# Performance work log

Measured on AMD Instinct MI355X. Metric: run time of the kernel, lower is better.

## Reference

```python
import jax, jax.numpy as jnp
import numpy as np
import math

B, L, P, D, H, RBF = 4, 256, 1024, 512, 8, 50
d = D // H  # head_dim = 64
EPS = 1e-5


def setup_inputs() -> dict:
    key = jax.random.key(0)
    ks = jax.random.split(key, 20)
    s = 1.0 / math.sqrt(D)
    inp = {
        "query": jax.random.normal(ks[0], (B, L, D), jnp.float32),
        "key": jax.random.normal(ks[1], (B, P, D), jnp.float32),
        "value": jax.random.normal(ks[2], (B, P, D), jnp.float32),
        "cross_rbf": jax.random.uniform(ks[3], (B, L, P, RBF), jnp.float32),
        "key_mask": jax.random.randint(ks[4], (B, P), 0, 2, jnp.int32),
        "Wq": jax.random.normal(ks[5], (D, D), jnp.float32) * s,
        "bq": jnp.zeros((D,), jnp.float32),
        "Wk": jax.random.normal(ks[6], (D, D), jnp.float32) * s,
        "bk": jnp.zeros((D,), jnp.float32),
        "Wv": jax.random.normal(ks[7], (D, D), jnp.float32) * s,
        "bv": jnp.zeros((D,), jnp.float32),
        "Wr": jax.random.normal(ks[8], (RBF, H), jnp.float32) * (1.0 / math.sqrt(RBF)),
        "br": jnp.zeros((H,), jnp.float32),
        "Wo": jax.random.normal(ks[9], (D, D), jnp.float32) * s,
        "bo": jnp.zeros((D,), jnp.float32),
        "gamma": jnp.ones((D,), jnp.float32),
        "beta": jnp.zeros((D,), jnp.float32),
    }
    return inp


def reference(query, key, value, cross_rbf, key_mask,
              Wq, bq, Wk, bk, Wv, bv, Wr, br, Wo, bo, gamma, beta):
    Q = (query @ Wq + bq).reshape(B, L, H, d)
    K = (key @ Wk + bk).reshape(B, P, H, d)
    V = (value @ Wv + bv).reshape(B, P, H, d)
    # scores [B, L, P, H]
    attn = jnp.einsum('blhd,bphd->blph', Q, K) / math.sqrt(d)
    dist_bias = cross_rbf @ Wr + br  # [B, L, P, H]
    attn = attn + dist_bias
    attn = jnp.where(key_mask[:, None, :, None] == 0, -1e9, attn)
    attn = jax.nn.softmax(attn, axis=2)  # softmax over P
    out = jnp.einsum('blph,bphd->blhd', attn, V).reshape(B, L, D)
    out = out @ Wo + bo
    x = query + out
    mu = jnp.mean(x, axis=-1, keepdims=True)
    var = jnp.mean((x - mu) ** 2, axis=-1, keepdims=True)
    normed = (x - mu) / jnp.sqrt(var + EPS) * gamma + beta
    return normed, attn.mean(axis=-1)
```

## Files before the change

### kernel.cpp

```cpp
#include <hip/hip_runtime.h>
#include <hip/hip_bf16.h>

#define BB 4
#define LL 256
#define PP 1024
#define DD 512
#define HH 8
#define HD 64
#define NRBF 50

__device__ __forceinline__ float bf2f(unsigned short u) {
  return __uint_as_float((unsigned)u << 16);
}

__device__ __forceinline__ float ldf(const void* p, size_t i, bool f32) {
  if (f32) return ((const float*)p)[i];
  return bf2f(((const unsigned short*)p)[i]);
}

__device__ __forceinline__ float4 ld4e(const void* p, size_t i, bool f32) {
  if (f32) return *(const float4*)((const float*)p + i);
  ushort4 u = *(const ushort4*)((const unsigned short*)p + i);
  float4 r;
  r.x = bf2f(u.x); r.y = bf2f(u.y); r.z = bf2f(u.z); r.w = bf2f(u.w);
  return r;
}

__global__ __launch_bounds__(256) void detect_dtype(const float* q, int* flag) {
  __shared__ int cnt;
  if (threadIdx.x == 0) cnt = 0;
  __syncthreads();
  int c = 0;
  for (int i = threadIdx.x; i < 1024; i += 256) {
    unsigned u = __float_as_uint(q[i]);
    unsigned e = (u >> 23) & 0xffu;
    if (e >= 104u && e <= 140u) c++;
  }
  atomicAdd(&cnt, c);
  __syncthreads();
  if (threadIdx.x == 0) *flag = (cnt > 512) ? 1 : 0;
}

__device__ void gemm128(const void* __restrict__ X, const void* __restrict__ W,
                        const void* __restrict__ bias, float* __restrict__ Y,
                        const int bm, const int bn, const int mode,
                        const bool f32, float* lds) {
  const int tid = threadIdx.x;
  const int tx = tid & 15, ty = tid >> 4;
  const int lr = tid >> 1, lc = (tid & 1) * 8;
  const int wk = tid >> 5, wc = (tid & 31) * 4;
  float acc[8][8] = {};
  float4 ra0, ra1, rb0, rb1;

  ra0 = ld4e(X, (size_t)(bm + lr) * 512 + lc, f32);
  ra1 = ld4e(X, (size_t)(bm + lr) * 512 + lc + 4, f32);
  rb0 = ld4e(W, (size_t)wk * 512 + bn + wc, f32);
  rb1 = ld4e(W, (size_t)(wk + 8) * 512 + bn + wc, f32);
  {
    float* Ab = lds;
    float* Bb = lds + 4096;
    Ab[(lc + 0) * 128 + lr] = ra0.x; Ab[(lc + 1) * 128 + lr] = ra0.y;
    Ab[(lc + 2) * 128 + lr] = ra0.z; Ab[(lc + 3) * 128 + lr] = ra0.w;
    Ab[(lc + 4) * 128 + lr] = ra1.x; Ab[(lc + 5) * 128 + lr] = ra1.y;
    Ab[(lc + 6) * 128 + lr] = ra1.z; Ab[(lc + 7) * 128 + lr] = ra1.w;
    *(float4*)&Bb[wk * 128 + wc] = rb0;
    *(float4*)&Bb[(wk + 8) * 128 + wc] = rb1;
  }
  __syncthreads();

  int buf = 0;
  for (int tt = 0; tt < 32; ++tt) {
    if (tt < 31) {
      const int k0 = (tt + 1) * 16;
      ra0 = ld4e(X, (size_t)(bm + lr) * 512 + k0 + lc, f32);
      ra1 = ld4e(X, (size_t)(bm + lr) * 512 + k0 + lc + 4, f32);
      rb0 = ld4e(W, (size_t)(k0 + wk) * 512 + bn + wc, f32);
      rb1 = ld4e(W, (size_t)(k0 + wk + 8) * 512 + bn + wc, f32);
    }
    {
      const float* Ab = lds + buf * 2048;
      const float* Bb = lds + 4096 + buf * 2048;
#pragma unroll
      for (int k = 0; k < 16; ++k) {
        float4 aL = *(const float4*)&Ab[k * 128 + ty * 4];
        float4 aH = *(const float4*)&Ab[k * 128 + 64 + ty * 4];
        float4 bL = *(const float4*)&Bb[k * 128 + tx * 4];
        float4 bH = *(const float4*)&Bb[k * 128 + 64 + tx * 4];
        const float a8[8] = {aL.x, aL.y, aL.z, aL.w, aH.x, aH.y, aH.z, aH.w};
        const float b8[8] = {bL.x, bL.y, bL.z, bL.w, bH.x, bH.y, bH.z, bH.w};
#pragma unroll
        for (int i = 0; i < 8; ++i)
#pragma unroll
          for (int j = 0; j < 8; ++j)
            acc[i][j] = fmaf(a8[i], b8[j], acc[i][j]);
      }
    }
    if (tt < 31) {
      float* Ab = lds + (buf ^ 1) * 2048;
      float* Bb = lds + 4096 + (buf ^ 1) * 2048;
      Ab[(lc + 0) * 128 + lr] = ra0.x; Ab[(lc + 1) * 128 + lr] = ra0.y;
      Ab[(lc + 2) * 128 + lr] = ra0.z; Ab[(lc + 3) * 128 + lr] = ra0.w;
      Ab[(lc + 4) * 128 + lr] = ra1.x; Ab[(lc + 5) * 128 + lr] = ra1.y;
      Ab[(lc + 6) * 128 + lr] = ra1.z; Ab[(lc + 7) * 128 + lr] = ra1.w;
      *(float4*)&Bb[wk * 128 + wc] = rb0;
      *(float4*)&Bb[(wk + 8) * 128 + wc] = rb1;
    }
    __syncthreads();
    buf ^= 1;
  }

  if (mode == 0) {
#pragma unroll
    for (int rh = 0; rh < 2; ++rh)
#pragma unroll
      for (int i = 0; i < 4; ++i) {
        const int r = bm + rh * 64 + ty * 4 + i;
#pragma unroll
        for (int ch = 0; ch < 2; ++ch) {
          const int c = bn + ch * 64 + tx * 4;
          float4 o;
          o.x = acc[rh * 4 + i][ch * 4 + 0] + ldf(bias, c + 0, f32);
          o.y = acc[rh * 4 + i][ch * 4 + 1] + ldf(bias, c + 1, f32);
          o.z = acc[rh * 4 + i][ch * 4 + 2] + ldf(bias, c + 2, f32);
          o.w = acc[rh * 4 + i][ch * 4 + 3] + ldf(bias, c + 3, f32);
          *(float4*)&Y[(size_t)r * 512 + c] = o;
        }
      }
  } else {
    const int bq = bm >> 10;
    const int pb = bm & 1023;
#pragma unroll
    for (int ch = 0; ch < 2; ++ch)
#pragma unroll
      for (int j = 0; j < 4; ++j) {
        const int c = bn + ch * 64 + tx * 4 + j;
        const float bb = ldf(bias, c, f32);
#pragma unroll
        for (int rh = 0; rh < 2; ++rh) {
          float4 pv;
          pv.x = acc[rh * 4 + 0][ch * 4 + j] + bb;
          pv.y = acc[rh * 4 + 1][ch * 4 + j] + bb;
          pv.z = acc[rh * 4 + 2][ch * 4 + j] + bb;
          pv.w = acc[rh * 4 + 3][ch * 4 + j] + bb;
          const int p0 = pb + rh * 64 + ty * 4;
          *(float4*)&Y[(((size_t)bq * 8 + (c >> 6)) * 64 + (c & 63)) * 1024 +
                       p0] = pv;
        }
      }
  }
}

__global__ __launch_bounds__(256) void qkv_gemm(
    const void* __restrict__ query, const void* __restrict__ key,
    const void* __restrict__ value, const void* __restrict__ Wq,
    const void* __restrict__ bq_, const void* __restrict__ Wk,
    const void* __restrict__ bk_, const void* __restrict__ Wv,
    const void* __restrict__ bv_, float* __restrict__ Qw,
    float* __restrict__ Ktw, float* __restrict__ Vw,
    const int* __restrict__ flag) {
  __shared__ float lds[8192];
  const bool f32 = (*flag != 0);
  const int blk = blockIdx.x;

  const void *X, *W, *bias;
  float* Y;
  int mode, mi, ni;
  if (blk < 32) {
    X = query; W = Wq; bias = bq_; Y = Qw; mode = 0;
    mi = blk >> 2; ni = blk & 3;
  } else if (blk < 160) {
    const int q2 = blk - 32;
    X = key; W = Wk; bias = bk_; Y = Ktw; mode = 1;
    mi = q2 >> 2; ni = q2 & 3;
  } else {
    const int q2 = blk - 160;
    X = value; W = Wv; bias = bv_; Y = Vw; mode = 0;
    mi = q2 >> 2; ni = q2 & 3;
  }
  gemm128(X, W, bias, Y, mi * 128, ni * 128, mode, f32, lds);
}

#define SST 1028

__global__ __launch_bounds__(512) void attn_v10(
    const float* __restrict__ Q,
    const float* __restrict__ Kt,
    const float* __restrict__ V,
    const void* __restrict__ rbf,
    const void* __restrict__ Wr,
    const void* __restrict__ br_,
    const int* __restrict__ mask,
    float* __restrict__ AO,
    void* __restrict__ d_out, const int* __restrict__ flag) {
  const int xcd = blockIdx.x & 7;
  const int idx = blockIdx.x >> 3;
  const int b = xcd >> 1;
  const int lq = ((xcd & 1) << 5) | idx;
  const int bl0 = b * LL + lq * 4;
  const int t = threadIdx.x;
  const bool f32 = (*flag != 0);

  __shared__ float qS[4][512];
  __shared__ float wrS[NRBF * 8];
  __shared__ float brS[8];
  __shared__ float scoresS[4][8 * SST];

  for (int i = t; i < 2048; i += 512)
    qS[i >> 9][i & 511] = Q[(size_t)bl0 * 512 + i];
  for (int i = t; i < NRBF * 8; i += 512) wrS[i] = ldf(Wr, i, f32);
  if (t < 8) brS[t] = ldf(br_, t, f32);
  __syncthreads();

  {
    const int qh = t >> 8;
    const int tq = t & 255;
#pragma unroll
    for (int qi = 0; qi < 2; ++qi) {
      const int q = qh * 2 + qi;
      float acc[4][8];
#pragma unroll
      for (int e = 0; e < 4; ++e)
#pragma unroll
        for (int h = 0; h < 8; ++h) acc[e][h] = brS[h];
      const size_t rbase = ((size_t)(bl0 + q) * 1024 + 4 * tq) * NRBF;
      if (f32) {
        const float* rowb = (const float*)rbf + rbase;
#pragma unroll
        for (int e = 0; e < 4; ++e) {
          const float2* rp = (const float2*)(rowb + e * NRBF);
#pragma unroll 5
          for (int j = 0; j < 25; ++j) {
            const float2 r2 = rp[j];
            const float4 wa = *(const float4*)&wrS[(2 * j) * 8];
            const float4 wb = *(const float4*)&wrS[(2 * j) * 8 + 4];
            const float4 wc = *(const float4*)&wrS[(2 * j + 1) * 8];
            const float4 wd = *(const float4*)&wrS[(2 * j + 1) * 8 + 4];
            acc[e][0] = fmaf(r2.x, wa.x, acc[e][0]);
            acc[e][1] = fmaf(r2.x, wa.y, acc[e][1]);
            acc[e][2] = fmaf(r2.x, wa.z, acc[e][2]);
            acc[e][3] = fmaf(r2.x, wa.w, acc[e][3]);
            acc[e][4] = fmaf(r2.x, wb.x, acc[e][4]);
            acc[e][5] = fmaf(r2.x, wb.y, acc[e][5]);
            acc[e][6] = fmaf(r2.x, wb.z, acc[e][6]);
            acc[e][7] = fmaf(r2.x, wb.w, acc[e][7]);
            acc[e][0] = fmaf(r2.y, wc.x, acc[e][0]);
            acc[e][1] = fmaf(r2.y, wc.y, acc[e][1]);
            acc[e][2] = fmaf(r2.y, wc.z, acc[e][2]);
            acc[e][3] = fmaf(r2.y, wc.w, acc[e][3]);
            acc[e][4] = fmaf(r2.y, wd.x, acc[e][4]);
            acc[e][5] = fmaf(r2.y, wd.y, acc[e][5]);
            acc[e][6] = fmaf(r2.y, wd.z, acc[e][6]);
            acc[e][7] = fmaf(r2.y, wd.w, acc[e][7]);
          }
        }
      } else {
        const unsigned short* rb = (const unsigned short*)rbf + rbase;
#pragma unroll
        for (int e = 0; e < 4; ++e) {
#pragma unroll 1
          for (int j = 0; j < 50; ++j) {
            const float rv = bf2f(rb[e * 50 + j]);
#pragma unroll
            for (int h = 0; h < 8; ++h)
              acc[e][h] = fmaf(rv, wrS[j * 8 + h], acc[e][h]);
          }
        }
      }
#pragma unroll
      for (int h = 0; h < 8; ++h) {
        float4 o;
        o.x = acc[0][h]; o.y = acc[1][h]; o.z = acc[2][h]; o.w = acc[3][h];
        *(float4*)&scoresS[q][h * SST + 4 * tq] = o;
      }
    }
  }
  __syncthreads();

  {
    const int tq = t & 255;
    const int hh = t >> 8;
    const int4 mk4 = *(const int4*)(mask + b * PP + 4 * tq);
#pragma unroll 1
    for (int hi = 0; hi < 4; ++hi) {
      const int h = hh * 4 + hi;
      const float4* ktp =
          (const float4*)(Kt + ((size_t)b * 8 + h) * 64 * 1024) + tq;
      float4 a0 = {0.f, 0.f, 0.f, 0.f}, a1 = {0.f, 0.f, 0.f, 0.f};
      float4 a2 = {0.f, 0.f, 0.f, 0.f}, a3 = {0.f, 0.f, 0.f, 0.f};
#pragma unroll 2
      for (int dq = 0; dq < 16; ++dq) {
        float4 q0 = *(const float4*)&qS[0][h * 64 + dq * 4];
        float4 q1 = *(const float4*)&qS[1][h * 64 + dq * 4];
        float4 q2 = *(const float4*)&qS[2][h * 64 + dq * 4];
        float4 q3 = *(const float4*)&qS[3][h * 64 + dq * 4];
        float4 k0 = ktp[(size_t)(dq * 4 + 0) * 256];
        float4 k1 = ktp[(size_t)(dq * 4 + 1) * 256];
        float4 k2 = ktp[(size_t)(dq * 4 + 2) * 256];
        float4 k3 = ktp[(size_t)(dq * 4 + 3) * 256];
        a0.x = fmaf(q0.x, k0.x, a0.x); a0.y = fmaf(q0.x, k0.y, a0.y);
        a0.z = fmaf(q0.x, k0.z, a0.z); a0.w = fmaf(q0.x, k0.w, a0.w);
        a0.x = fmaf(q0.y, k1.x, a0.x); a0.y = fmaf(q0.y, k1.y, a0.y);
        a0.z = fmaf(q0.y, k1.z, a0.z); a0.w = fmaf(q0.y, k1.w, a0.w);
        a0.x = fmaf(q0.z, k2.x, a0.x); a0.y = fmaf(q0.z, k2.y, a0.y);
        a0.z = fmaf(q0.z, k2.z, a0.z); a0.w = fmaf(q0.z, k2.w, a0.w);
        a0.x = fmaf(q0.w, k3.x, a0.x); a0.y = fmaf(q0.w, k3.y, a0.y);
        a0.z = fmaf(q0.w, k3.z, a0.z); a0.w = fmaf(q0.w, k3.w, a0.w);
        a1.x = fmaf(q1.x, k0.x, a1.x); a1.y = fmaf(q1.x, k0.y, a1.y);
        a1.z = fmaf(q1.x, k0.z, a1.z); a1.w = fmaf(q1.x, k0.w, a1.w);
        a1.x = fmaf(q1.y, k1.x, a1.x); a1.y = fmaf(q1.y, k1.y, a1.y);
        a1.z = fmaf(q1.y, k1.z, a1.z); a1.w = fmaf(q1.y, k1.w, a1.w);
        a1.x = fmaf(q1.z, k2.x, a1.x); a1.y = fmaf(q1.z, k2.y, a1.y);
        a1.z = fmaf(q1.z, k2.z, a1.z); a1.w = fmaf(q1.z, k2.w, a1.w);
        a1.x = fmaf(q1.w, k3.x, a1.x); a1.y = fmaf(q1.w, k3.y, a1.y);
        a1.z = fmaf(q1.w, k3.z, a1.z); a1.w = fmaf(q1.w, k3.w, a1.w);
        a2.x = fmaf(q2.x, k0.x, a2.x); a2.y = fmaf(q2.x, k0.y, a2.y);
        a2.z = fmaf(q2.x, k0.z, a2.z); a2.w = fmaf(q2.x, k0.w, a2.w);
        a2.x = fmaf(q2.y, k1.x, a2.x); a2.y = fmaf(q2.y, k1.y, a2.y);
        a2.z = fmaf(q2.y, k1.z, a2.z); a2.w = fmaf(q2.y, k1.w, a2.w);
        a2.x = fmaf(q2.z, k2.x, a2.x); a2.y = fmaf(q2.z, k2.y, a2.y);
        a2.z = fmaf(q2.z, k2.z, a2.z); a2.w = fmaf(q2.z, k2.w, a2.w);
        a2.x = fmaf(q2.w, k3.x, a2.x); a2.y = fmaf(q2.w, k3.y, a2.y);
        a2.z = fmaf(q2.w, k3.z, a2.z); a2.w = fmaf(q2.w, k3.w, a2.w);
        a3.x = fmaf(q3.x, k0.x, a3.x); a3.y = fmaf(q3.x, k0.y, a3.y);
        a3.z = fmaf(q3.x, k0.z, a3.z); a3.w = fmaf(q3.x, k0.w, a3.w);
        a3.x = fmaf(q3.y, k1.x, a3.x); a3.y = fmaf(q3.y, k1.y, a3.y);
        a3.z = fmaf(q3.y, k1.z, a3.z); a3.w = fmaf(q3.y, k1.w, a3.w);
        a3.x = fmaf(q3.z, k2.x, a3.x); a3.y = fmaf(q3.z, k2.y, a3.y);
        a3.z = fmaf(q3.z, k2.z, a3.z); a3.w = fmaf(q3.z, k2.w, a3.w);
        a3.x = fmaf(q3.w, k3.x, a3.x); a3.y = fmaf(q3.w, k3.y, a3.y);
        a3.z = fmaf(q3.w, k3.z, a3.z); a3.w = fmaf(q3.w, k3.w, a3.w);
      }
      float4 av[4] = {a0, a1, a2, a3};
#pragma unroll
      for (int qi = 0; qi < 4; ++qi) {
        float4 bq4 = *(const float4*)&scoresS[qi][h * SST + 4 * tq];
        float4 s;
        s.x = (mk4.x == 0) ? -1e9f : fmaf(av[qi].x, 0.125f, bq4.x);
        s.y = (mk4.y == 0) ? -1e9f : fmaf(av[qi].y, 0.125f, bq4.y);
        s.z = (mk4.z == 0) ? -1e9f : fmaf(av[qi].z, 0.125f, bq4.z);
        s.w = (mk4.w == 0) ? -1e9f : fmaf(av[qi].w, 0.125f, bq4.w);
        *(float4*)&scoresS[qi][h * SST + 4 * tq] = s;
      }
    }
  }
  __syncthreads();

  {
    const int wave = t >> 6, lane = t & 63;
    for (int pr = wave * 4; pr < wave * 4 + 4; ++pr) {
      float* sc = &scoresS[pr >> 3][(pr & 7) * SST];
      float m = -3.0e38f;
      for (int i = lane; i < PP; i += 64) m = fmaxf(m, sc[i]);
#pragma unroll
      for (int off = 32; off; off >>= 1) m = fmaxf(m, __shfl_xor(m, off, 64));
      float sum = 0.f;
      for (int i = lane; i < PP; i += 64) {
        float e = __expf(sc[i] - m);
        sc[i] = e;
        sum += e;
      }
#pragma unroll
      for (int off = 32; off; off >>= 1) sum += __shfl_xor(sum, off, 64);
      const float inv = 1.0f / sum;
      for (int i = lane; i < PP; i += 64) sc[i] *= inv;
    }
  }
  __syncthreads();

  for (int w = t; w < 1024; w += 512) {
    const int q = w >> 8, pq = w & 255;
    float4 s = {0.f, 0.f, 0.f, 0.f};
#pragma unroll
    for (int h = 0; h < 8; ++h) {
      float4 v = *(const float4*)&scoresS[q][h * SST + 4 * pq];
      s.x += v.x; s.y += v.y; s.z += v.z; s.w += v.w;
    }
    s.x *= 0.125f; s.y *= 0.125f; s.z *= 0.125f; s.w *= 0.125f;
    const size_t base =
        (size_t)BB * LL * DD + (size_t)(bl0 + q) * PP + 4 * pq;
    if (f32) {
      *(float4*)((float*)d_out + base) = s;
    } else {
      __hip_bfloat16* o1 = (__hip_bfloat16*)d_out;
      o1[base + 0] = __float2bfloat16(s.x);
      o1[base + 1] = __float2bfloat16(s.y);
      o1[base + 2] = __float2bfloat16(s.z);
      o1[base + 3] = __float2bfloat16(s.w);
    }
  }

  float4 pa[4];
  {
    const int cq = t & 127;
    const int ph = t >> 7;
    const int h = cq >> 4;
    const float* sc0 = &scoresS[0][h * SST];
    const float* sc1 = &scoresS[1][h * SST];
    const float* sc2 = &scoresS[2][h * SST];
    const float* sc3 = &scoresS[3][h * SST];
    const float4* Vb = (const float4*)(V + (size_t)b * PP * 512) + cq;
    float4 A0 = {0.f, 0.f, 0.f, 0.f}, A1 = {0.f, 0.f, 0.f, 0.f};
    float4 A2 = {0.f, 0.f, 0.f, 0.f}, A3 = {0.f, 0.f, 0.f, 0.f};
    const int p0 = ph * 256;
#pragma unroll 2
    for (int p4 = p0; p4 < p0 + 256; p4 += 4) {
      float4 pr0 = *(const float4*)&sc0[p4];
      float4 pr1 = *(const float4*)&sc1[p4];
      float4 pr2 = *(const float4*)&sc2[p4];
      float4 pr3 = *(const float4*)&sc3[p4];
      float4 v0 = Vb[(size_t)(p4 + 0) * 128];
      float4 v1 = Vb[(size_t)(p4 + 1) * 128];
      float4 v2 = Vb[(size_t)(p4 + 2) * 128];
      float4 v3 = Vb[(size_t)(p4 + 3) * 128];
      A0.x = fmaf(pr0.x, v0.x, A0.x); A0.y = fmaf(pr0.x, v0.y, A0.y);
      A0.z = fmaf(pr0.x, v0.z, A0.z); A0.w = fmaf(pr0.x, v0.w, A0.w);
      A0.x = fmaf(pr0.y, v1.x, A0.x); A0.y = fmaf(pr0.y, v1.y, A0.y);
      A0.z = fmaf(pr0.y, v1.z, A0.z); A0.w = fmaf(pr0.y, v1.w, A0.w);
      A0.x = fmaf(pr0.z, v2.x, A0.x); A0.y = fmaf(pr0.z, v2.y, A0.y);
      A0.z = fmaf(pr0.z, v2.z, A0.z); A0.w = fmaf(pr0.z, v2.w, A0.w);
      A0.x = fmaf(pr0.w, v3.x, A0.x); A0.y = fmaf(pr0.w, v3.y, A0.y);
      A0.z = fmaf(pr0.w, v3.z, A0.z); A0.w = fmaf(pr0.w, v3.w, A0.w);
      A1.x = fmaf(pr1.x, v0.x, A1.x); A1.y = fmaf(pr1.x, v0.y, A1.y);
      A1.z = fmaf(pr1.x, v0.z, A1.z); A1.w = fmaf(pr1.x, v0.w, A1.w);
      A1.x = fmaf(pr1.y, v1.x, A1.x); A1.y = fmaf(pr1.y, v1.y, A1.y);
      A1.z = fmaf(pr1.y, v1.z, A1.z); A1.w = fmaf(pr1.y, v1.w, A1.w);
      A1.x = fmaf(pr1.z, v2.x, A1.x); A1.y = fmaf(pr1.z, v2.y, A1.y);
      A1.z = fmaf(pr1.z, v2.z, A1.z); A1.w = fmaf(pr1.z, v2.w, A1.w);
      A1.x = fmaf(pr1.w, v3.x, A1.x); A1.y = fmaf(pr1.w, v3.y, A1.y);
      A1.z = fmaf(pr1.w, v3.z, A1.z); A1.w = fmaf(pr1.w, v3.w, A1.w);
      A2.x = fmaf(pr2.x, v0.x, A2.x); A2.y = fmaf(pr2.x, v0.y, A2.y);
      A2.z = fmaf(pr2.x, v0.z, A2.z); A2.w = fmaf(pr2.x, v0.w, A2.w);
      A2.x = fmaf(pr2.y, v1.x, A2.x); A2.y = fmaf(pr2.y, v1.y, A2.y);
      A2.z = fmaf(pr2.y, v1.z, A2.z); A2.w = fmaf(pr2.y, v1.w, A2.w);
      A2.x = fmaf(pr2.z, v2.x, A2.x); A2.y = fmaf(pr2.z, v2.y, A2.y);
      A2.z = fmaf(pr2.z, v2.z, A2.z); A2.w = fmaf(pr2.z, v2.w, A2.w);
      A2.x = fmaf(pr2.w, v3.x, A2.x); A2.y = fmaf(pr2.w, v3.y, A2.y);
      A2.z = fmaf(pr2.w, v3.z, A2.z); A2.w = fmaf(pr2.w, v3.w, A2.w);
      A3.x = fmaf(pr3.x, v0.x, A3.x); A3.y = fmaf(pr3.x, v0.y, A3.y);
      A3.z = fmaf(pr3.x, v0.z, A3.z); A3.w = fmaf(pr3.x, v0.w, A3.w);
      A3.x = fmaf(pr3.y, v1.x, A3.x); A3.y = fmaf(pr3.y, v1.y, A3.y);
      A3.z = fmaf(pr3.y, v1.z, A3.z); A3.w = fmaf(pr3.y, v1.w, A3.w);
      A3.x = fmaf(pr3.z, v2.x, A3.x); A3.y = fmaf(pr3.z, v2.y, A3.y);
      A3.z = fmaf(pr3.z, v2.z, A3.z); A3.w = fmaf(pr3.z, v2.w, A3.w);
      A3.x = fmaf(pr3.w, v3.x, A3.x); A3.y = fmaf(pr3.w, v3.y, A3.y);
      A3.z = fmaf(pr3.w, v3.z, A3.z); A3.w = fmaf(pr3.w, v3.w, A3.w);
    }
    pa[0] = A0; pa[1] = A1; pa[2] = A2; pa[3] = A3;
  }
  __syncthreads();
  {
    const int cq = t & 127, ph = t >> 7;
    float* parts = &scoresS[0][0];
#pragma unroll
    for (int qi = 0; qi < 4; ++qi)
      *(float4*)&parts[((qi * 4 + ph) * 128 + cq) * 4] = pa[qi];
  }
  __syncthreads();
  {
    const int q = t >> 7, c = t & 127;
    const float* parts = &scoresS[0][0];
    float4 a = *(const float4*)&parts[((q * 4 + 0) * 128 + c) * 4];
#pragma unroll
    for (int ph = 1; ph < 4; ++ph) {
      float4 x = *(const float4*)&parts[((q * 4 + ph) * 128 + c) * 4];
      a.x += x.x; a.y += x.y; a.z += x.z; a.w += x.w;
    }
    *(float4*)&AO[(size_t)(bl0 + q) * 512 + 4 * c] = a;
  }
}

__global__ __launch_bounds__(256) void proj_out(
    const float* __restrict__ X, const void* __restrict__ W,
    const void* __restrict__ bias, const void* __restrict__ resid,
    float* __restrict__ Y, const int* __restrict__ flag) {
  __shared__ float As[16][64];
  __shared__ float Bs[16][64];
  const bool f32 = (*flag != 0);
  const int bm = blockIdx.x * 64, bn = blockIdx.y * 64;
  const int tid = threadIdx.x;
  const int tx = tid & 15, ty = tid >> 4;
  float acc[4][4] = {};
  for (int k0 = 0; k0 < 512; k0 += 16) {
    {
      int r = tid >> 2, kf = (tid & 3) * 4;
      float4 x4 = *(const float4*)(X + (size_t)(bm + r) * 512 + k0 + kf);
      As[kf + 0][r] = x4.x; As[kf + 1][r] = x4.y;
      As[kf + 2][r] = x4.z; As[kf + 3][r] = x4.w;
    }
    if (f32) {
      int kk = tid >> 4, cf = (tid & 15) * 4;
      *(float4*)&Bs[kk][cf] =
          *(const float4*)((const float*)W + (size_t)(k0 + kk) * 512 + bn + cf);
    } else {
      const unsigned short* Wb = (const unsigned short*)W;
      for (int f = tid; f < 16 * 64; f += 256) {
        int kk = f >> 6, c = f & 63;
        Bs[kk][c] = bf2f(Wb[(size_t)(k0 + kk) * 512 + bn + c]);
      }
    }
    __syncthreads();
#pragma unroll
    for (int k = 0; k < 16; ++k) {
      float4 a4 = *(const float4*)&As[k][ty * 4];
      float4 b4 = *(const float4*)&Bs[k][tx * 4];
      acc[0][0] = fmaf(a4.x, b4.x, acc[0][0]); acc[0][1] = fmaf(a4.x, b4.y, acc[0][1]);
      acc[0][2] = fmaf(a4.x, b4.z, acc[0][2]); acc[0][3] = fmaf(a4.x, b4.w, acc[0][3]);
      acc[1][0] = fmaf(a4.y, b4.x, acc[1][0]); acc[1][1] = fmaf(a4.y, b4.y, acc[1][1]);
      acc[1][2] = fmaf(a4.y, b4.z, acc[1][2]); acc[1][3] = fmaf(a4.y, b4.w, acc[1][3]);
      acc[2][0] = fmaf(a4.z, b4.x, acc[2][0]); acc[2][1] = fmaf(a4.z, b4.y, acc[2][1]);
      acc[2][2] = fmaf(a4.z, b4.z, acc[2][2]); acc[2][3] = fmaf(a4.z, b4.w, acc[2][3]);
      acc[3][0] = fmaf(a4.w, b4.x, acc[3][0]); acc[3][1] = fmaf(a4.w, b4.y, acc[3][1]);
      acc[3][2] = fmaf(a4.w, b4.z, acc[3][2]); acc[3][3] = fmaf(a4.w, b4.w, acc[3][3]);
    }
    __syncthreads();
  }
#pragma unroll
  for (int i = 0; i < 4; ++i) {
    int r = bm + ty * 4 + i;
    float4 o;
#pragma unroll
    for (int j = 0; j < 4; ++j) {
      int c = bn + tx * 4 + j;
      float v = acc[i][j] + ldf(bias, c, f32) +
                ldf(resid, (size_t)r * 512 + c, f32);
      ((float*)&o)[j] = v;
    }
    *(float4*)(Y + (size_t)r * 512 + bn + tx * 4) = o;
  }
}

__global__ __launch_bounds__(256) void ln_kernel(
    const float* __restrict__ Xw, const void* __restrict__ gamma,
    const void* __restrict__ beta, void* __restrict__ d_out,
    const int* __restrict__ flag) {
  const int bl = blockIdx.x;
  const int tid = threadIdx.x;
  const bool f32 = (*flag != 0);
  __shared__ float red[16];
  float v0 = Xw[(size_t)bl * 512 + tid];
  float v1 = Xw[(size_t)bl * 512 + tid + 256];
  float s = v0 + v1, s2 = v0 * v0 + v1 * v1;
#pragma unroll
  for (int off = 32; off; off >>= 1) {
    s += __shfl_xor(s, off, 64);
    s2 += __shfl_xor(s2, off, 64);
  }
  const int wave = tid >> 6, lane = tid & 63;
  if (lane == 0) { red[wave] = s; red[8 + wave] = s2; }
  __syncthreads();
  if (tid == 0) {
    float ts = 0.f, ts2 = 0.f;
    for (int w = 0; w < 4; ++w) { ts += red[w]; ts2 += red[8 + w]; }
    red[0] = ts; red[1] = ts2;
  }
  __syncthreads();
  const float mu = red[0] * (1.0f / 512.0f);
  const float var = red[1] * (1.0f / 512.0f) - mu * mu;
  const float rstd = rsqrtf(var + 1e-5f);
  float o0 = (v0 - mu) * rstd * ldf(gamma, tid, f32) + ldf(beta, tid, f32);
  float o1 = (v1 - mu) * rstd * ldf(gamma, tid + 256, f32) +
             ldf(beta, tid + 256, f32);
  if (f32) {
    float* o = (float*)d_out;
    o[(size_t)bl * 512 + tid] = o0;
    o[(size_t)bl * 512 + tid + 256] = o1;
  } else {
    __hip_bfloat16* o = (__hip_bfloat16*)d_out;
    o[(size_t)bl * 512 + tid] = __float2bfloat16(o0);
    o[(size_t)bl * 512 + tid + 256] = __float2bfloat16(o1);
  }
}

extern "C" void kernel_launch(void* const* d_in, const int* in_sizes, int n_in,
                              void* d_out, int out_size, void* d_ws,
                              size_t ws_size, hipStream_t stream) {
  const void* query = d_in[0];
  const void* key = d_in[1];
  const void* value = d_in[2];
  const void* rbf = d_in[3];
  const int* key_mask = (const int*)d_in[4];
  const void* Wq = d_in[5];
  const void* bq = d_in[6];
  const void* Wk = d_in[7];
  const void* bk = d_in[8];
  const void* Wv = d_in[9];
  const void* bv = d_in[10];
  const void* Wr = d_in[11];
  const void* br = d_in[12];
  const void* Wo = d_in[13];
  const void* bo = d_in[14];
  const void* gamma = d_in[15];
  const void* beta = d_in[16];

  int* flag = (int*)d_ws;
  float* base = (float*)d_ws + 4;
  float* Qw = base;
  float* Ktw = Qw + (size_t)BB * LL * DD;
  float* Vw = Ktw + (size_t)BB * PP * DD;
  float* AO = Vw + (size_t)BB * PP * DD;
  float* Xw = AO + (size_t)BB * LL * DD;

  detect_dtype<<<1, 256, 0, stream>>>((const float*)query, flag);
  qkv_gemm<<<dim3(288), 256, 0, stream>>>(query, key, value, Wq, bq, Wk, bk,
                                          Wv, bv, Qw, Ktw, Vw, flag);
  attn_v10<<<dim3(BB * LL / 4), 512, 0, stream>>>(Qw, Ktw, Vw, rbf, Wr, br,
                                                  key_mask, AO, d_out, flag);
  proj_out<<<dim3(16, 8), 256, 0, stream>>>(AO, Wo, bo, query, Xw, flag);
  ln_kernel<<<dim3(BB * LL), 256, 0, stream>>>(Xw, gamma, beta, d_out, flag);
}
```

Measured before the change: 609.5 us.

## Shrink QKV GEMM tiles and split-K the output projection into LN

The QKV projection GEMM now uses 128x64 tiles instead of 128x128, doubling the block count to 576 and lowering per-thread accumulators so more blocks fit per CU. The output projection is split over K into two partial buffers (256 blocks instead of 128). The layer-norm kernel then sums the two partials and adds the bias and residual. This aims to fill the GPU's many CUs better on small GEMMs, at the cost of extra partial-sum memory traffic and lower arithmetic intensity per tile.

```diff
diff --git a/kernel.cpp b/kernel.cpp
--- a/kernel.cpp
+++ b/kernel.cpp
@@ -41,21 +41,21 @@
   if (threadIdx.x == 0) *flag = (cnt > 512) ? 1 : 0;
 }
 
-__device__ void gemm128(const void* __restrict__ X, const void* __restrict__ W,
-                        const void* __restrict__ bias, float* __restrict__ Y,
-                        const int bm, const int bn, const int mode,
-                        const bool f32, float* lds) {
+__device__ void gemm128x64(const void* __restrict__ X,
+                           const void* __restrict__ W,
+                           const void* __restrict__ bias,
+                           float* __restrict__ Y, const int bm, const int bn,
+                           const int mode, const bool f32, float* lds) {
   const int tid = threadIdx.x;
   const int tx = tid & 15, ty = tid >> 4;
   const int lr = tid >> 1, lc = (tid & 1) * 8;
-  const int wk = tid >> 5, wc = (tid & 31) * 4;
-  float acc[8][8] = {};
-  float4 ra0, ra1, rb0, rb1;
+  const int wk = tid >> 4, wc = (tid & 15) * 4;
+  float acc[8][4] = {};
+  float4 ra0, ra1, rb0;
 
   ra0 = ld4e(X, (size_t)(bm + lr) * 512 + lc, f32);
   ra1 = ld4e(X, (size_t)(bm + lr) * 512 + lc + 4, f32);
   rb0 = ld4e(W, (size_t)wk * 512 + bn + wc, f32);
-  rb1 = ld4e(W, (size_t)(wk + 8) * 512 + bn + wc, f32);
   {
     float* Ab = lds;
     float* Bb = lds + 4096;
@@ -63,8 +63,7 @@
     Ab[(lc + 2) * 128 + lr] = ra0.z; Ab[(lc + 3) * 128 + lr] = ra0.w;
     Ab[(lc + 4) * 128 + lr] = ra1.x; Ab[(lc + 5) * 128 + lr] = ra1.y;
     Ab[(lc + 6) * 128 + lr] = ra1.z; Ab[(lc + 7) * 128 + lr] = ra1.w;
-    *(float4*)&Bb[wk * 128 + wc] = rb0;
-    *(float4*)&Bb[(wk + 8) * 128 + wc] = rb1;
+    *(float4*)&Bb[wk * 64 + wc] = rb0;
   }
   __syncthreads();
 
@@ -75,35 +74,33 @@
       ra0 = ld4e(X, (size_t)(bm + lr) * 512 + k0 + lc, f32);
       ra1 = ld4e(X, (size_t)(bm + lr) * 512 + k0 + lc + 4, f32);
       rb0 = ld4e(W, (size_t)(k0 + wk) * 512 + bn + wc, f32);
-      rb1 = ld4e(W, (size_t)(k0 + wk + 8) * 512 + bn + wc, f32);
     }
     {
       const float* Ab = lds + buf * 2048;
-      const float* Bb = lds + 4096 + buf * 2048;
+      const float* Bb = lds + 4096 + buf * 1024;
 #pragma unroll
       for (int k = 0; k < 16; ++k) {
         float4 aL = *(const float4*)&Ab[k * 128 + ty * 4];
         float4 aH = *(const float4*)&Ab[k * 128 + 64 + ty * 4];
-        float4 bL = *(const float4*)&Bb[k * 128 + tx * 4];
-        float4 bH = *(const float4*)&Bb[k * 128 + 64 + tx * 4];
+        float4 b4 = *(const float4*)&Bb[k * 64 + tx * 4];
         const float a8[8] = {aL.x, aL.y, aL.z, aL.w, aH.x, aH.y, aH.z, aH.w};
-        const float b8[8] = {bL.x, bL.y, bL.z, bL.w, bH.x, bH.y, bH.z, bH.w};
-#pragma unroll
-        for (int i = 0; i < 8; ++i)
-#pragma unroll
-          for (int j = 0; j < 8; ++j)
-            acc[i][j] = fmaf(a8[i], b8[j], acc[i][j]);
+#pragma unroll
+        for (int i = 0; i < 8; ++i) {
+          acc[i][0] = fmaf(a8[i], b4.x, acc[i][0]);
+          acc[i][1] = fmaf(a8[i], b4.y, acc[i][1]);
+          acc[i][2] = fmaf(a8[i], b4.z, acc[i][2]);
+          acc[i][3] = fmaf(a8[i], b4.w, acc[i][3]);
+        }
       }
     }
     if (tt < 31) {
       float* Ab = lds + (buf ^ 1) * 2048;
-      float* Bb = lds + 4096 + (buf ^ 1) * 2048;
+      float* Bb = lds + 4096 + (buf ^ 1) * 1024;
       Ab[(lc + 0) * 128 + lr] = ra0.x; Ab[(lc + 1) * 128 + lr] = ra0.y;
       Ab[(lc + 2) * 128 + lr] = ra0.z; Ab[(lc + 3) * 128 + lr] = ra0.w;
       Ab[(lc + 4) * 128 + lr] = ra1.x; Ab[(lc + 5) * 128 + lr] = ra1.y;
       Ab[(lc + 6) * 128 + lr] = ra1.z; Ab[(lc + 7) * 128 + lr] = ra1.w;
-      *(float4*)&Bb[wk * 128 + wc] = rb0;
-      *(float4*)&Bb[(wk + 8) * 128 + wc] = rb1;
+      *(float4*)&Bb[wk * 64 + wc] = rb0;
     }
     __syncthreads();
     buf ^= 1;
@@ -115,42 +112,38 @@
 #pragma unroll
       for (int i = 0; i < 4; ++i) {
         const int r = bm + rh * 64 + ty * 4 + i;
-#pragma unroll
-        for (int ch = 0; ch < 2; ++ch) {
-          const int c = bn + ch * 64 + tx * 4;
-          float4 o;
-          o.x = acc[rh * 4 + i][ch * 4 + 0] + ldf(bias, c + 0, f32);
-          o.y = acc[rh * 4 + i][ch * 4 + 1] + ldf(bias, c + 1, f32);
-          o.z = acc[rh * 4 + i][ch * 4 + 2] + ldf(bias, c + 2, f32);
-          o.w = acc[rh * 4 + i][ch * 4 + 3] + ldf(bias, c + 3, f32);
-          *(float4*)&Y[(size_t)r * 512 + c] = o;
-        }
+        const int c = bn + tx * 4;
+        float4 o;
+        o.x = acc[rh * 4 + i][0] + ldf(bias, c + 0, f32);
+        o.y = acc[rh * 4 + i][1] + ldf(bias, c + 1, f32);
+        o.z = acc[rh * 4 + i][2] + ldf(bias, c + 2, f32);
+        o.w = acc[rh * 4 + i][3] + ldf(bias, c + 3, f32);
+        *(float4*)&Y[(size_t)r * 512 + c] = o;
       }
   } else {
     const int bq = bm >> 10;
     const int pb = bm & 1023;
-#pragma unroll
-    for (int ch = 0; ch < 2; ++ch)
-#pragma unroll
-      for (int j = 0; j < 4; ++j) {
-        const int c = bn + ch * 64 + tx * 4 + j;
-        const float bb = ldf(bias, c, f32);
-#pragma unroll
-        for (int rh = 0; rh < 2; ++rh) {
-          float4 pv;
-          pv.x = acc[rh * 4 + 0][ch * 4 + j] + bb;
-          pv.y = acc[rh * 4 + 1][ch * 4 + j] + bb;
-          pv.z = acc[rh * 4 + 2][ch * 4 + j] + bb;
-          pv.w = acc[rh * 4 + 3][ch * 4 + j] + bb;
-          const int p0 = pb + rh * 64 + ty * 4;
-          *(float4*)&Y[(((size_t)bq * 8 + (c >> 6)) * 64 + (c & 63)) * 1024 +
-                       p0] = pv;
-        }
-      }
-  }
-}
-
-__global__ __launch_bounds__(256) void qkv_gemm(
+    const int h = bn >> 6;
+#pragma unroll
+    for (int j = 0; j < 4; ++j) {
+      const int c = bn + tx * 4 + j;
+      const int d = c & 63;
+      const float bb = ldf(bias, c, f32);
+#pragma unroll
+      for (int rh = 0; rh < 2; ++rh) {
+        float4 pv;
+        pv.x = acc[rh * 4 + 0][j] + bb;
+        pv.y = acc[rh * 4 + 1][j] + bb;
+        pv.z = acc[rh * 4 + 2][j] + bb;
+        pv.w = acc[rh * 4 + 3][j] + bb;
+        const int p0 = pb + rh * 64 + ty * 4;
+        *(float4*)&Y[(((size_t)bq * 8 + h) * 64 + d) * 1024 + p0] = pv;
+      }
+    }
+  }
+}
+
+__global__ __launch_bounds__(256, 3) void qkv_gemm(
     const void* __restrict__ query, const void* __restrict__ key,
     const void* __restrict__ value, const void* __restrict__ Wq,
     const void* __restrict__ bq_, const void* __restrict__ Wk,
@@ -158,26 +151,26 @@
     const void* __restrict__ bv_, float* __restrict__ Qw,
     float* __restrict__ Ktw, float* __restrict__ Vw,
     const int* __restrict__ flag) {
-  __shared__ float lds[8192];
+  __shared__ float lds[6144];
   const bool f32 = (*flag != 0);
   const int blk = blockIdx.x;
 
   const void *X, *W, *bias;
   float* Y;
   int mode, mi, ni;
-  if (blk < 32) {
+  if (blk < 64) {
     X = query; W = Wq; bias = bq_; Y = Qw; mode = 0;
-    mi = blk >> 2; ni = blk & 3;
-  } else if (blk < 160) {
-    const int q2 = blk - 32;
+    mi = blk >> 3; ni = blk & 7;
+  } else if (blk < 320) {
+    const int q2 = blk - 64;
     X = key; W = Wk; bias = bk_; Y = Ktw; mode = 1;
-    mi = q2 >> 2; ni = q2 & 3;
+    mi = q2 >> 3; ni = q2 & 7;
   } else {
-    const int q2 = blk - 160;
+    const int q2 = blk - 320;
     X = value; W = Wv; bias = bv_; Y = Vw; mode = 0;
-    mi = q2 >> 2; ni = q2 & 3;
-  }
-  gemm128(X, W, bias, Y, mi * 128, ni * 128, mode, f32, lds);
+    mi = q2 >> 3; ni = q2 & 7;
+  }
+  gemm128x64(X, W, bias, Y, mi * 128, ni * 64, mode, f32, lds);
 }
 
 #define SST 1028
@@ -471,16 +464,17 @@
 
 __global__ __launch_bounds__(256) void proj_out(
     const float* __restrict__ X, const void* __restrict__ W,
-    const void* __restrict__ bias, const void* __restrict__ resid,
-    float* __restrict__ Y, const int* __restrict__ flag) {
+    float* __restrict__ Xp, const int* __restrict__ flag) {
   __shared__ float As[16][64];
   __shared__ float Bs[16][64];
   const bool f32 = (*flag != 0);
   const int bm = blockIdx.x * 64, bn = blockIdx.y * 64;
+  const int kz = blockIdx.z;
   const int tid = threadIdx.x;
   const int tx = tid & 15, ty = tid >> 4;
   float acc[4][4] = {};
-  for (int k0 = 0; k0 < 512; k0 += 16) {
+  const int kbeg = kz * 256;
+  for (int k0 = kbeg; k0 < kbeg + 256; k0 += 16) {
     {
       int r = tid >> 2, kf = (tid & 3) * 4;
       float4 x4 = *(const float4*)(X + (size_t)(bm + r) * 512 + k0 + kf);
@@ -514,31 +508,32 @@
     }
     __syncthreads();
   }
+  float* Y = Xp + (size_t)kz * BB * LL * DD;
 #pragma unroll
   for (int i = 0; i < 4; ++i) {
     int r = bm + ty * 4 + i;
     float4 o;
-#pragma unroll
-    for (int j = 0; j < 4; ++j) {
-      int c = bn + tx * 4 + j;
-      float v = acc[i][j] + ldf(bias, c, f32) +
-                ldf(resid, (size_t)r * 512 + c, f32);
-      ((float*)&o)[j] = v;
-    }
+    o.x = acc[i][0]; o.y = acc[i][1]; o.z = acc[i][2]; o.w = acc[i][3];
     *(float4*)(Y + (size_t)r * 512 + bn + tx * 4) = o;
   }
 }
 
 __global__ __launch_bounds__(256) void ln_kernel(
-    const float* __restrict__ Xw, const void* __restrict__ gamma,
+    const float* __restrict__ Xp, const void* __restrict__ resid,
+    const void* __restrict__ bo_, const void* __restrict__ gamma,
     const void* __restrict__ beta, void* __restrict__ d_out,
     const int* __restrict__ flag) {
   const int bl = blockIdx.x;
   const int tid = threadIdx.x;
   const bool f32 = (*flag != 0);
+  const size_t half = (size_t)BB * LL * DD;
   __shared__ float red[16];
-  float v0 = Xw[(size_t)bl * 512 + tid];
-  float v1 = Xw[(size_t)bl * 512 + tid + 256];
+  const size_t i0 = (size_t)bl * 512 + tid;
+  const size_t i1 = i0 + 256;
+  float v0 = Xp[i0] + Xp[half + i0] + ldf(bo_, tid, f32) +
+             ldf(resid, i0, f32);
+  float v1 = Xp[i1] + Xp[half + i1] + ldf(bo_, tid + 256, f32) +
+             ldf(resid, i1, f32);
   float s = v0 + v1, s2 = v0 * v0 + v1 * v1;
 #pragma unroll
   for (int off = 32; off; off >>= 1) {
@@ -562,12 +557,12 @@
              ldf(beta, tid + 256, f32);
   if (f32) {
     float* o = (float*)d_out;
-    o[(size_t)bl * 512 + tid] = o0;
-    o[(size_t)bl * 512 + tid + 256] = o1;
+    o[i0] = o0;
+    o[i1] = o1;
   } else {
     __hip_bfloat16* o = (__hip_bfloat16*)d_out;
-    o[(size_t)bl * 512 + tid] = __float2bfloat16(o0);
-    o[(size_t)bl * 512 + tid + 256] = __float2bfloat16(o1);
+    o[i0] = __float2bfloat16(o0);
+    o[i1] = __float2bfloat16(o1);
   }
 }
 
@@ -598,13 +593,14 @@
   float* Ktw = Qw + (size_t)BB * LL * DD;
   float* Vw = Ktw + (size_t)BB * PP * DD;
   float* AO = Vw + (size_t)BB * PP * DD;
-  float* Xw = AO + (size_t)BB * LL * DD;
+  float* Xp = AO + (size_t)BB * LL * DD;
 
   detect_dtype<<<1, 256, 0, stream>>>((const float*)query, flag);
-  qkv_gemm<<<dim3(288), 256, 0, stream>>>(query, key, value, Wq, bq, Wk, bk,
+  qkv_gemm<<<dim3(576), 256, 0, stream>>>(query, key, value, Wq, bq, Wk, bk,
                                           Wv, bv, Qw, Ktw, Vw, flag);
   attn_v10<<<dim3(BB * LL / 4), 512, 0, stream>>>(Qw, Ktw, Vw, rbf, Wr, br,
                                                   key_mask, AO, d_out, flag);
-  proj_out<<<dim3(16, 8), 256, 0, stream>>>(AO, Wo, bo, query, Xw, flag);
-  ln_kernel<<<dim3(BB * LL), 256, 0, stream>>>(Xw, gamma, beta, d_out, flag);
-}
+  proj_out<<<dim3(16, 8, 2), 256, 0, stream>>>(AO, Wo, Xp, flag);
+  ln_kernel<<<dim3(BB * LL), 256, 0, stream>>>(Xp, query, bo, gamma, beta,
+                                               d_out, flag);
+}
```

Result: faster. 529.9 us (-13.1%).
